# Kernel tuning notes

Hardware: AMD Instinct MI355X
Metric: run time of the kernel (lower is better)

The kernel has to match this reference:

```python
import jax, jax.numpy as jnp
import numpy as np
import math

NPAD = 100      # npadding
NLAYERS = 4     # transformer_num_layers
NHEAD = 8       # transformer_nhead


def _posenc(T, d):
    pos = jnp.arange(T, dtype=jnp.float32)[:, None]
    div = jnp.exp(jnp.arange(0, d, 2, dtype=jnp.float32) * (-(math.log(1000.0) / d)))
    pe = jnp.zeros((T, d), jnp.float32)
    pe = pe.at[:, 0::2].set(jnp.sin(pos * div))
    pe = pe.at[:, 1::2].set(jnp.cos(pos * div))
    return pe


def _ln(x, g, b):
    m = x.mean(-1, keepdims=True)
    v = ((x - m) ** 2).mean(-1, keepdims=True)
    return (x - m) / jnp.sqrt(v + 1e-5) * g + b


def conv_individual(Y, kernel, npadding):
    # Y: (B,N,Ttot); kernel: (ntau,N). Causal zero-pad then FFT conv (faithful to source).
    B, N, Ttot = Y.shape
    kernel = jnp.concatenate([jnp.zeros((1, N), kernel.dtype), kernel], axis=0)
    ntau = kernel.shape[0]
    nn = Ttot + ntau - 1
    Yf = jnp.fft.fft(Y, n=nn, axis=2)                 # (B,N,nn) complex
    Kf = jnp.fft.fft(kernel.T, n=nn, axis=-1)          # (N,nn)
    c = jnp.fft.ifft(Yf * Kf[None], axis=2).real
    c = jnp.where(jnp.abs(c) < 1e-5, 0.0, c)           # ad-hoc small-value zeroing from source
    return c[:, :, :Ttot][:, :, npadding:]             # (B,N,T)


def conv_subspace(Y, kernel, npadding):
    # Y: (B,N,Ttot); kernel: (ntau,S) -> G: (B,N,S,T)
    B, N, Ttot = Y.shape
    k = kernel[None]                                   # (1,ntau,S)
    k = jnp.concatenate([jnp.zeros((1, 1, k.shape[2]), jnp.float32), k], axis=1)
    ntau = k.shape[1]
    nn = Ttot + ntau - 1
    Yf = jnp.fft.fft(Y, n=nn, axis=2)[..., None]       # (B,N,nn,1)
    Kf = jnp.fft.fft(k, n=nn, axis=1)[None]            # (1,1,nn,S)
    G = jnp.fft.ifft(Yf * Kf, axis=2).real             # (B,N,nn,S)
    G = jnp.where(jnp.abs(G) < 1e-5, 0.0, G)
    G = G[:, :, :Ttot, :][:, :, npadding:, :]
    return jnp.swapaxes(G, -1, -2)                     # (B,N,S,T)


def _encoder(x, Wqkv, bqkv, Wo, bo, ln1_g, ln1_b, W1, b1, W2, b2, ln2_g, ln2_b):
    B, T, D = x.shape
    hd = D // NHEAD
    for l in range(NLAYERS):
        qkv = x @ Wqkv[l] + bqkv[l]                    # (B,T,3D)
        q, k, v = jnp.split(qkv, 3, axis=-1)
        q = q.reshape(B, T, NHEAD, hd)
        k = k.reshape(B, T, NHEAD, hd)
        v = v.reshape(B, T, NHEAD, hd)
        scores = jnp.einsum('bthd,bshd->bhts', q, k) / jnp.sqrt(jnp.float32(hd))
        attn = jax.nn.softmax(scores, axis=-1)
        o = jnp.einsum('bhts,bshd->bthd', attn, v).reshape(B, T, D)
        x = _ln(x + (o @ Wo[l] + bo[l]), ln1_g[l], ln1_b[l])
        ff = jax.nn.gelu(x @ W1[l] + b1[l], approximate=False) @ W2[l] + b2[l]
        x = _ln(x + ff, ln2_g[l], ln2_b[l])
    return x


def reference(Y, token_W, token_b, Wqkv, bqkv, Wo, bo, ln1_g, ln1_b, W1, b1, W2, b2,
              ln2_g, ln2_b, toL_W, toL_b, dec_W1, dec_b1, dec_W2, dec_b2,
              stimulus_basis, readout_W, coupling_W, coupling_basis, self_kernel):
    B, N, Ttot = Y.shape
    T = Ttot - NPAD
    D = token_W.shape[1]
    # token conversion over time (seq dim = time)
    x = jnp.swapaxes(Y[:, :, NPAD:], 1, 2) @ token_W + token_b   # (B,T,D)
    x = x + _posenc(T, D)[None]
    x = _encoder(x, Wqkv, bqkv, Wo, bo, ln1_g, ln1_b, W1, b1, W2, b2, ln2_g, ln2_b)
    pooled = x.mean(axis=1)                                      # (B,D)
    h = pooled @ toL_W + toL_b                                   # (B,2Z)
    Z = h.shape[1] // 2
    z = h[:, :Z]                                                 # mu (sample_latent=False)
    # stimulus decoder (2-layer MLP)
    coeffs = jax.nn.relu(z @ dec_W1 + dec_b1) @ dec_W2 + dec_b2  # (B, NF*NB)
    NB = stimulus_basis.shape[1]
    NF = coeffs.shape[1] // NB
    coeffs = coeffs.reshape(B, NF, NB)
    sti_lat = jnp.einsum('bfk,tk->bft', coeffs, stimulus_basis)  # (B,NF,T)
    sti = jnp.einsum('nf,bft->bnt', readout_W, sti_lat)          # (B,N,T)
    # coupling via FFT causal conv into subspaces
    G = conv_subspace(Y, coupling_basis, NPAD)                   # (B,N,S,T)
    cpl = jnp.einsum('ns,bnst->bnt', coupling_W, G)
    # self-history FFT causal conv
    slf = conv_individual(Y, self_kernel, NPAD)
    return sti + cpl + slf                                       # log firing rate (B,N,T)


def setup_inputs() -> dict:
    key = jax.random.key(0)
    ks = jax.random.split(key, 30)
    B, N, Ttot = 16, 256, 1100
    D, FF, Zdim = 256, 1024, 64
    NB, NF, S, NTAU = 30, 4, 4, 20   # NF = narea*stimulus_nfactor = 2*2
    T = Ttot - NPAD
    sc = 0.02
    inp = {
        'Y': jax.random.uniform(ks[0], (B, N, Ttot), jnp.float32),
        'token_W': jax.random.normal(ks[1], (N, D), jnp.float32) * sc,
        'token_b': jnp.zeros((D,), jnp.float32),
        'Wqkv': jax.random.normal(ks[2], (NLAYERS, D, 3 * D), jnp.float32) * sc,
        'bqkv': jnp.zeros((NLAYERS, 3 * D), jnp.float32),
        'Wo': jax.random.normal(ks[3], (NLAYERS, D, D), jnp.float32) * sc,
        'bo': jnp.zeros((NLAYERS, D), jnp.float32),
        'ln1_g': jnp.ones((NLAYERS, D), jnp.float32),
        'ln1_b': jnp.zeros((NLAYERS, D), jnp.float32),
        'W1': jax.random.normal(ks[4], (NLAYERS, D, FF), jnp.float32) * sc,
        'b1': jnp.zeros((NLAYERS, FF), jnp.float32),
        'W2': jax.random.normal(ks[5], (NLAYERS, FF, D), jnp.float32) * sc,
        'b2': jnp.zeros((NLAYERS, D), jnp.float32),
        'ln2_g': jnp.ones((NLAYERS, D), jnp.float32),
        'ln2_b': jnp.zeros((NLAYERS, D), jnp.float32),
        'toL_W': jax.random.normal(ks[6], (D, 2 * Zdim), jnp.float32) * sc,
        'toL_b': jnp.zeros((2 * Zdim,), jnp.float32),
        'dec_W1': jax.random.normal(ks[7], (Zdim, 2 * Zdim), jnp.float32) * sc,
        'dec_b1': jnp.zeros((2 * Zdim,), jnp.float32),
        'dec_W2': jax.random.normal(ks[8], (2 * Zdim, NB * NF), jnp.float32) * sc * 0.001,
        'dec_b2': jnp.zeros((NB * NF,), jnp.float32),
        'stimulus_basis': jax.random.normal(ks[9], (T, NB), jnp.float32),
        'readout_W': jax.random.normal(ks[10], (N, NF), jnp.float32) * sc,
        'coupling_W': jax.random.normal(ks[11], (N, S), jnp.float32) * sc,
        'coupling_basis': jax.random.normal(ks[12], (NTAU, S), jnp.float32) * 0.1,
        'self_kernel': jax.random.normal(ks[13], (NTAU, N), jnp.float32) * 0.1,
    }
    return inp
```

## Files before the change

kernel.cpp:

```cpp
#include <hip/hip_runtime.h>
#include <math.h>

#define TT_   1000
#define TTOT_ 1100
#define NPAD_ 100
#define DD_   256
#define NN_   256

#define X_OFF    0u
#define XB_OFF   4096000u
#define O_OFF    6144000u
#define R_OFF    8192000u
#define BIG_OFF  12288000u
#define WT_OFF   20480000u
#define PE_OFF   22085632u
#define PP_OFF   22341632u
#define PL_OFF   (PP_OFF + 32768u)
#define CF_OFF   (PL_OFF + 4096u)
#define CB_OFF   (CF_OFF + 1920u)
#define BQ_OFF   (CB_OFF + 5120u)
#define STL_OFF  (BQ_OFF + 3072u)

#define SC2_ 0.25503902254649546f

typedef __attribute__((ext_vector_type(8))) short s16x8;
typedef __attribute__((ext_vector_type(4))) float f32x4;
typedef __attribute__((ext_vector_type(16))) float f32x16;
typedef __attribute__((ext_vector_type(4))) unsigned u32x4;

__device__ inline short f2bf(float f) {
    unsigned u = __float_as_uint(f);
    u += 0x7fffu + ((u >> 16) & 1u);
    return (short)(u >> 16);
}
__device__ inline float exp2i(float x) {
    float r; asm("v_exp_f32 %0, %1" : "=v"(r) : "v"(x)); return r;
}

__device__ inline void gl_lds16(const short* g, short* l) {
    __builtin_amdgcn_global_load_lds(
        (const __attribute__((address_space(1))) void*)g,
        (__attribute__((address_space(3))) void*)l, 16, 0, 0);
}

__global__ __launch_bounds__(256) void wtr_k(const float* __restrict__ in,
                                             short* __restrict__ out, int K, int N,
                                             int qrows, float qs)
{
    __shared__ float t[32][33];
    const int n0 = blockIdx.x * 32, k0 = blockIdx.y * 32;
    in  += (size_t)blockIdx.z * K * N;
    out += (size_t)blockIdx.z * K * N;
    const int tx = threadIdx.x & 31, ty = threadIdx.x >> 5;
    #pragma unroll
    for (int i = 0; i < 4; ++i)
        t[ty + 8 * i][tx] = in[(size_t)(k0 + ty + 8 * i) * N + n0 + tx];
    __syncthreads();
    #pragma unroll
    for (int i = 0; i < 4; ++i) {
        const int row = n0 + ty + 8 * i;
        float f = t[tx][ty + 8 * i];
        if (row < qrows) f *= qs;
        out[(size_t)row * K + k0 + tx] = f2bf(f);
    }
}

__global__ __launch_bounds__(256) void ytr_k(const float* __restrict__ Y,
                                             short* __restrict__ out)
{
    __shared__ float t[32][33];
    const int b = blockIdx.z;
    const int t0 = blockIdx.x * 32, n0 = blockIdx.y * 32;
    const int tx = threadIdx.x & 31, ty = threadIdx.x >> 5;
    #pragma unroll
    for (int i = 0; i < 4; ++i) {
        const int tt = t0 + tx;
        t[ty + 8 * i][tx] = (tt < TT_)
            ? Y[((size_t)(b * NN_ + n0 + ty + 8 * i)) * TTOT_ + NPAD_ + tt] : 0.f;
    }
    __syncthreads();
    #pragma unroll
    for (int i = 0; i < 4; ++i) {
        const int tt = t0 + ty + 8 * i;
        if (tt < TT_)
            out[((size_t)(b * TT_ + tt)) * NN_ + n0 + tx] = f2bf(t[tx][ty + 8 * i]);
    }
}

__global__ void pe_k(float* __restrict__ PE)
{
    const int t = blockIdx.x, d = threadIdx.x;
    const float div = __expf(-(float)(d & ~1) * 0.0269834190585241f);
    const float ang = (float)t * div;
    PE[t * 256 + d] = (d & 1) ? cosf(ang) : sinf(ang);
}

__global__ void bscale_k(const float* __restrict__ in, float* __restrict__ out)
{
    const int i = blockIdx.x * 256 + threadIdx.x;
    if (i < 3072) {
        const int col = i % 768;
        out[i] = in[i] * ((col < 256) ? SC2_ : 1.f);
    }
}

template<int OUTBF, int ACT, int RES, int DUAL>
__global__ __launch_bounds__(256) void bgemm_k(const short* __restrict__ A,
                                               const short* __restrict__ Bt,
                                               const float* __restrict__ bias,
                                               const float* __restrict__ resid,
                                               void* __restrict__ Cout,
                                               short* __restrict__ Cb,
                                               int M, int N, int K, int nby)
{
    __shared__ short As[64 * 64];
    __shared__ short Bs[128 * 64];
    const int tid = threadIdx.x;

    const int nwg = gridDim.x;
    int gid = blockIdx.x;
    {
        const int q = nwg >> 3, r = nwg & 7;
        const int x = gid & 7, idx = gid >> 3;
        gid = (x < r ? x * (q + 1) : r * (q + 1) + (x - r) * q) + idx;
    }
    const int bx = gid / nby, by = gid - bx * nby;
    const int m0 = bx * 64, n0 = by * 128;

    const int wv = tid >> 6, lane = tid & 63;
    const int wr = wv >> 1, wc = wv & 1;
    const int l15 = lane & 15, lg = lane >> 4;

    f32x4 acc[2][4];
    #pragma unroll
    for (int i = 0; i < 2; ++i)
        #pragma unroll
        for (int j = 0; j < 4; ++j) acc[i][j] = (f32x4){0.f, 0.f, 0.f, 0.f};

    const int nt = K >> 6;
    for (int t = 0; t < nt; ++t) {
        __syncthreads();
        const int k0 = t << 6;
        #pragma unroll
        for (int i = 0; i < 2; ++i) {
            const int cid = i * 256 + tid;
            const int r = cid >> 3, c = cid & 7;
            gl_lds16(A + (size_t)(m0 + r) * K + k0 + ((c ^ (r & 7)) * 8), As + cid * 8);
        }
        #pragma unroll
        for (int i = 0; i < 4; ++i) {
            const int cid = i * 256 + tid;
            const int r = cid >> 3, c = cid & 7;
            gl_lds16(Bt + (size_t)(n0 + r) * K + k0 + ((c ^ (r & 7)) * 8), Bs + cid * 8);
        }
        __syncthreads();

        #pragma unroll
        for (int ks = 0; ks < 2; ++ks) {
            s16x8 af[2], bf[4];
            #pragma unroll
            for (int mi = 0; mi < 2; ++mi) {
                const int row = wr * 32 + mi * 16 + l15;
                const int ch = ks * 4 + lg;
                af[mi] = *(const s16x8*)(As + row * 64 + ((ch ^ (row & 7)) * 8));
            }
            #pragma unroll
            for (int ni = 0; ni < 4; ++ni) {
                const int col = wc * 64 + ni * 16 + l15;
                const int ch = ks * 4 + lg;
                bf[ni] = *(const s16x8*)(Bs + col * 64 + ((ch ^ (col & 7)) * 8));
            }
            #pragma unroll
            for (int mi = 0; mi < 2; ++mi)
                #pragma unroll
                for (int ni = 0; ni < 4; ++ni)
                    acc[mi][ni] = __builtin_amdgcn_mfma_f32_16x16x32_bf16(
                        af[mi], bf[ni], acc[mi][ni], 0, 0, 0);
        }
    }

    #pragma unroll
    for (int mi = 0; mi < 2; ++mi) {
        #pragma unroll
        for (int ni = 0; ni < 4; ++ni) {
            const int col = n0 + wc * 64 + ni * 16 + l15;
            const float bv = bias[col];
            #pragma unroll
            for (int r = 0; r < 4; ++r) {
                const int row = m0 + wr * 32 + mi * 16 + lg * 4 + r;
                float v = acc[mi][ni][r] + bv;
                if (RES == 1) v += resid[(size_t)row * N + col];
                if (RES == 2) v += resid[(size_t)(row % 1000) * N + col];
                if (ACT) v = 0.5f * v * (1.0f + erff(v * 0.70710678118654752f));
                if (OUTBF) ((short*)Cout)[(size_t)row * N + col] = f2bf(v);
                else       ((float*)Cout)[(size_t)row * N + col] = v;
                if (DUAL)  Cb[(size_t)row * N + col] = f2bf(v);
            }
        }
    }
}

__global__ __launch_bounds__(256) void mattn_k(const short* __restrict__ qkv,
                                               short* __restrict__ o)
{
    int wg = blockIdx.x;
    wg = (wg & 7) * 128 + (wg >> 3);
    const int qt = wg & 7, h = (wg >> 3) & 7, b = wg >> 6;

    const int tid = threadIdx.x, wv = tid >> 6, lane = tid & 63;
    const int q31 = lane & 31, hi = lane >> 5;
    __shared__ short Ks[2][64 * 40];
    __shared__ short VT[2][32 * 72];

    const int q0w = qt * 128 + wv * 32;
    int qrow = q0w + q31; if (qrow > 999) qrow = 999;
    s16x8 bq[2];
    #pragma unroll
    for (int dh = 0; dh < 2; ++dh)
        bq[dh] = *(const s16x8*)(qkv + ((size_t)(b * TT_ + qrow)) * 768 + h * 32 + dh * 16 + hi * 8);

    f32x16 oacc;
    #pragma unroll
    for (int i = 0; i < 16; ++i) oacc[i] = 0.f;
    float lrun = 0.f;

    const int sr = tid >> 2, sc = tid & 3;
    s16x8 kreg, vreg;
    auto LOADT = [&](int kt) {
        int t = kt * 64 + sr; if (t > 999) t = 999;
        const short* src = qkv + ((size_t)(b * TT_ + t)) * 768 + 256 + h * 32;
        kreg = *(const s16x8*)(src + sc * 8);
        vreg = *(const s16x8*)(src + 256 + sc * 8);
    };
    auto WRITET = [&](int buf) {
        *(s16x8*)(&Ks[buf][sr * 40 + sc * 8]) = kreg;
        #pragma unroll
        for (int j = 0; j < 8; ++j)
            VT[buf][(sc * 8 + j) * 72 + (((sr >> 3) ^ sc) * 8) + (sr & 7)] = vreg[j];
    };

    LOADT(0); WRITET(0);
    __syncthreads();
    int cur = 0;

    for (int kt = 0; kt < 16; ++kt) {
        if (kt < 15) LOADT(kt + 1);

        f32x16 st[2];
        __builtin_amdgcn_s_setprio(1);
        #pragma unroll
        for (int kb = 0; kb < 2; ++kb) {
            s16x8 kf0 = *(const s16x8*)(&Ks[cur][(kb * 32 + q31) * 40 + hi * 8]);
            s16x8 kf1 = *(const s16x8*)(&Ks[cur][(kb * 32 + q31) * 40 + 16 + hi * 8]);
            f32x16 z;
            #pragma unroll
            for (int i = 0; i < 16; ++i) z[i] = 0.f;
            z = __builtin_amdgcn_mfma_f32_32x32x16_bf16(kf0, bq[0], z, 0, 0, 0);
            z = __builtin_amdgcn_mfma_f32_32x32x16_bf16(kf1, bq[1], z, 0, 0, 0);
            st[kb] = z;
        }
        __builtin_amdgcn_s_setprio(0);

        if (kt == 15) {
            #pragma unroll
            for (int kb = 0; kb < 2; ++kb)
                #pragma unroll
                for (int r = 0; r < 16; ++r) {
                    const int kloc = kb * 32 + (r & 3) + 8 * (r >> 2) + 4 * hi;
                    if (960 + kloc >= TT_) st[kb][r] = -1e30f;
                }
        }

        float sloc = 0.f;
        #pragma unroll
        for (int kb = 0; kb < 2; ++kb)
            #pragma unroll
            for (int r = 0; r < 16; ++r) {
                const float p = exp2i(st[kb][r]);
                st[kb][r] = p; sloc += p;
            }
        sloc += __shfl_xor(sloc, 32);
        lrun += sloc;

        unsigned wk[2][4][2];
        #pragma unroll
        for (int kb = 0; kb < 2; ++kb)
            #pragma unroll
            for (int a = 0; a < 4; ++a)
                #pragma unroll
                for (int h2 = 0; h2 < 2; ++h2) {
                    unsigned rr;
                    asm("v_cvt_pk_bf16_f32 %0, %1, %2"
                        : "=v"(rr)
                        : "v"(st[kb][4 * a + 2 * h2]), "v"(st[kb][4 * a + 2 * h2 + 1]));
                    wk[kb][a][h2] = rr;
                }

        #pragma unroll
        for (int ks = 0; ks < 4; ++ks) {
            const int kb = ks >> 1, qq = ks & 1;
            unsigned W[4];
            #pragma unroll
            for (int h2 = 0; h2 < 2; ++h2) {
                const unsigned send = hi ? wk[kb][2 * qq][h2] : wk[kb][2 * qq + 1][h2];
                const unsigned recv = __shfl_xor(send, 32);
                W[h2]     = hi ? recv : wk[kb][2 * qq][h2];
                W[2 + h2] = hi ? wk[kb][2 * qq + 1][h2] : recv;
            }
            u32x4 w4 = (u32x4){W[0], W[1], W[2], W[3]};
            s16x8 pb = __builtin_bit_cast(s16x8, w4);
            s16x8 vf = *(const s16x8*)(&VT[cur][q31 * 72 + (((2 * ks + hi) ^ (q31 >> 3)) * 8)]);
            __builtin_amdgcn_s_setprio(1);
            oacc = __builtin_amdgcn_mfma_f32_32x32x16_bf16(vf, pb, oacc, 0, 0, 0);
            __builtin_amdgcn_s_setprio(0);
        }

        if (kt < 15) WRITET(cur ^ 1);
        __syncthreads();
        cur ^= 1;
    }

    const int t = q0w + q31;
    if (t < TT_) {
        const float inv = 1.f / lrun;
        short* ob = o + ((size_t)(b * TT_ + t)) * 256 + h * 32;
        #pragma unroll
        for (int a = 0; a < 4; ++a) {
            unsigned w0, w1;
            asm("v_cvt_pk_bf16_f32 %0, %1, %2"
                : "=v"(w0) : "v"(oacc[4 * a + 0] * inv), "v"(oacc[4 * a + 1] * inv));
            asm("v_cvt_pk_bf16_f32 %0, %1, %2"
                : "=v"(w1) : "v"(oacc[4 * a + 2] * inv), "v"(oacc[4 * a + 3] * inv));
            const int d0 = 8 * a + 4 * hi;
            *(unsigned*)(ob + d0) = w0;
            *(unsigned*)(ob + d0 + 2) = w1;
        }
    }
}

__global__ __launch_bounds__(256) void ln_k(const float* __restrict__ in,
                                            const float* __restrict__ g,
                                            const float* __restrict__ b,
                                            float* __restrict__ out,
                                            short* __restrict__ outb)
{
    const int row = blockIdx.x * 4 + (threadIdx.x >> 6);
    const int lane = threadIdx.x & 63;
    const size_t base = (size_t)row * 256 + lane * 4;
    float4 v = *(const float4*)(in + base);
    float s = v.x + v.y + v.z + v.w;
    #pragma unroll
    for (int msk = 1; msk < 64; msk <<= 1) s += __shfl_xor(s, msk);
    const float mean = s * (1.f / 256.f);
    float4 d; d.x = v.x - mean; d.y = v.y - mean; d.z = v.z - mean; d.w = v.w - mean;
    float q = d.x * d.x + d.y * d.y + d.z * d.z + d.w * d.w;
    #pragma unroll
    for (int msk = 1; msk < 64; msk <<= 1) q += __shfl_xor(q, msk);
    const float rs = rsqrtf(q * (1.f / 256.f) + 1e-5f);
    const float4 g4 = *(const float4*)(g + lane * 4);
    const float4 b4 = *(const float4*)(b + lane * 4);
    float4 o4;
    o4.x = d.x * rs * g4.x + b4.x;
    o4.y = d.y * rs * g4.y + b4.y;
    o4.z = d.z * rs * g4.z + b4.z;
    o4.w = d.w * rs * g4.w + b4.w;
    *(float4*)(out + base) = o4;
    short4 s4;
    s4.x = f2bf(o4.x); s4.y = f2bf(o4.y); s4.z = f2bf(o4.z); s4.w = f2bf(o4.w);
    *(short4*)(outb + base) = s4;
}

__global__ __launch_bounds__(256) void pool_part_k(const float* __restrict__ X,
                                                   float* __restrict__ partial)
{
    const int b = blockIdx.x, seg = blockIdx.y, d = threadIdx.x;
    float s = 0.f;
    const int t0 = seg * 125;
    for (int t = t0; t < t0 + 125; ++t) s += X[((size_t)b * TT_ + t) * 256 + d];
    partial[(b * 8 + seg) * 256 + d] = s;
}
__global__ __launch_bounds__(256) void pool_red_k(const float* __restrict__ partial,
                                                  float* __restrict__ pooled)
{
    const int b = blockIdx.x, d = threadIdx.x;
    float s = 0.f;
    for (int k = 0; k < 8; ++k) s += partial[(b * 8 + k) * 256 + d];
    pooled[b * 256 + d] = s * (1.f / (float)TT_);
}

__global__ __launch_bounds__(128) void head_k(const float* __restrict__ pooled,
                                              const float* __restrict__ toLW,
                                              const float* __restrict__ toLb,
                                              const float* __restrict__ dW1,
                                              const float* __restrict__ db1,
                                              const float* __restrict__ dW2,
                                              const float* __restrict__ db2,
                                              float* __restrict__ coeffs)
{
    const int b = blockIdx.x, j = threadIdx.x;
    __shared__ float hs[64];
    __shared__ float hid[128];
    float a = toLb[j];
    for (int d = 0; d < 256; ++d) a += pooled[b * 256 + d] * toLW[d * 128 + j];
    if (j < 64) hs[j] = a;
    __syncthreads();
    float a2 = db1[j];
    for (int z = 0; z < 64; ++z) a2 += hs[z] * dW1[z * 128 + j];
    hid[j] = fmaxf(a2, 0.f);
    __syncthreads();
    if (j < 120) {
        float a3 = db2[j];
        for (int k = 0; k < 128; ++k) a3 += hid[k] * dW2[k * 120 + j];
        coeffs[b * 120 + j] = a3;
    }
}

__global__ void comb_k(const float* __restrict__ selfK,
                       const float* __restrict__ cplW,
                       const float* __restrict__ cplB,
                       float* __restrict__ comb)
{
    const int n = threadIdx.x;
    for (int ti = 0; ti < 20; ++ti) {
        float s = selfK[ti * 256 + n];
        #pragma unroll
        for (int si = 0; si < 4; ++si) s += cplW[n * 4 + si] * cplB[ti * 4 + si];
        comb[n * 20 + ti] = s;
    }
}

__global__ __launch_bounds__(256) void stilat_k(const float* __restrict__ SB,
                                                const float* __restrict__ coeffs,
                                                float* __restrict__ STL)
{
    const int bf = blockIdx.x;
    __shared__ float c[30];
    if (threadIdx.x < 30) c[threadIdx.x] = coeffs[(bf >> 2) * 120 + (bf & 3) * 30 + threadIdx.x];
    __syncthreads();
    for (int t = threadIdx.x; t < TT_; t += 256) {
        float acc = 0.f;
        const float* sp = SB + (size_t)t * 30;
        #pragma unroll
        for (int k = 0; k < 30; ++k) acc += c[k] * sp[k];
        STL[bf * TT_ + t] = acc;
    }
}

__global__ __launch_bounds__(256) void final_k(const float* __restrict__ Y,
                                               const float* __restrict__ STL,
                                               const float* __restrict__ roW,
                                               const float* __restrict__ comb,
                                               float* __restrict__ out)
{
    const int bx = blockIdx.x;
    const int ts = bx & 3, nc = (bx >> 2) & 31, b = bx >> 7;
    const int n0 = nc * 8, t0 = ts * 250;
    const int tid = threadIdx.x;
    __shared__ float rw[8][4], ck[8][20], yl[8][272];

    if (tid < 32) rw[tid >> 2][tid & 3] = roW[(n0 + (tid >> 2)) * 4 + (tid & 3)];
    if (tid >= 64 && tid < 224) {
        const int j = tid - 64;
        ck[j / 20][j % 20] = comb[(n0 + j / 20) * 20 + (j % 20)];
    }
    for (int j = tid; j < 2160; j += 256) {
        const int n = j / 270, jj = j - n * 270;
        yl[n][jj] = Y[((size_t)(b * 256 + n0 + n)) * TTOT_ + t0 + 80 + jj];
    }
    __syncthreads();

    if (tid < 250) {
        const int t = t0 + tid;
        float s4[4];
        #pragma unroll
        for (int f = 0; f < 4; ++f) s4[f] = STL[((size_t)b * 4 + f) * TT_ + t];
        #pragma unroll
        for (int n = 0; n < 8; ++n) {
            float acc = rw[n][0] * s4[0] + rw[n][1] * s4[1]
                      + rw[n][2] * s4[2] + rw[n][3] * s4[3];
            #pragma unroll
            for (int tau = 1; tau <= 20; ++tau)
                acc += ck[n][tau - 1] * yl[n][tid + 20 - tau];
            out[((size_t)(b * 256 + n0 + n)) * TT_ + t] = acc;
        }
    }
}

extern "C" void kernel_launch(void* const* d_in, const int* in_sizes, int n_in,
                              void* d_out, int out_size, void* d_ws, size_t ws_size,
                              hipStream_t stream)
{
    const float* Y      = (const float*)d_in[0];
    const float* tokW   = (const float*)d_in[1];
    const float* tokb   = (const float*)d_in[2];
    const float* Wqkv   = (const float*)d_in[3];
    const float* bqkv   = (const float*)d_in[4];
    const float* Wo     = (const float*)d_in[5];
    const float* bo     = (const float*)d_in[6];
    const float* ln1g   = (const float*)d_in[7];
    const float* ln1b   = (const float*)d_in[8];
    const float* W1     = (const float*)d_in[9];
    const float* b1     = (const float*)d_in[10];
    const float* W2     = (const float*)d_in[11];
    const float* b2     = (const float*)d_in[12];
    const float* ln2g   = (const float*)d_in[13];
    const float* ln2b   = (const float*)d_in[14];
    const float* toLW   = (const float*)d_in[15];
    const float* toLb   = (const float*)d_in[16];
    const float* dW1    = (const float*)d_in[17];
    const float* db1    = (const float*)d_in[18];
    const float* dW2    = (const float*)d_in[19];
    const float* db2    = (const float*)d_in[20];
    const float* SB     = (const float*)d_in[21];
    const float* roW    = (const float*)d_in[22];
    const float* cplW   = (const float*)d_in[23];
    const float* cplB   = (const float*)d_in[24];
    const float* selfK  = (const float*)d_in[25];

    float* ws  = (float*)d_ws;
    float* X   = ws + X_OFF;
    short* Xb  = (short*)(ws + XB_OFF);
    short* O   = (short*)(ws + O_OFF);
    float* R   = ws + R_OFF;
    short* BIG = (short*)(ws + BIG_OFF);
    short* WT  = (short*)(ws + WT_OFF);
    float* PE  = ws + PE_OFF;
    float* PP  = ws + PP_OFF;
    float* PL  = ws + PL_OFF;
    float* CF  = ws + CF_OFF;
    float* CB  = ws + CB_OFF;
    float* BQ  = ws + BQ_OFF;
    float* STL = ws + STL_OFF;

    short* WTqkv = WT;
    short* WTo   = WT + 786432;
    short* WTw1  = WT + 1048576;
    short* WTw2  = WT + 2097152;
    short* WTtok = WT + 3145728;
    short* Ybt   = BIG;

    wtr_k<<<dim3(24, 8, 4), 256, 0, stream>>>(Wqkv, WTqkv, 256, 768, 256, SC2_);
    wtr_k<<<dim3(8, 8, 4),  256, 0, stream>>>(Wo,   WTo,   256, 256, 0, 1.f);
    wtr_k<<<dim3(32, 8, 4), 256, 0, stream>>>(W1,   WTw1,  256, 1024, 0, 1.f);
    wtr_k<<<dim3(8, 32, 4), 256, 0, stream>>>(W2,   WTw2,  1024, 256, 0, 1.f);
    wtr_k<<<dim3(8, 8, 1),  256, 0, stream>>>(tokW, WTtok, 256, 256, 0, 1.f);
    bscale_k<<<12, 256, 0, stream>>>(bqkv, BQ);
    pe_k<<<1000, 256, 0, stream>>>(PE);
    ytr_k<<<dim3(32, 8, 16), 256, 0, stream>>>(Y, Ybt);

    bgemm_k<0, 0, 2, 1><<<500, 256, 0, stream>>>(
        Ybt, WTtok, tokb, PE, X, Xb, 16000, 256, 256, 2);

    for (int l = 0; l < 4; ++l) {
        bgemm_k<1, 0, 0, 0><<<1500, 256, 0, stream>>>(
            Xb, WTqkv + (size_t)l * 196608, BQ + l * 768, nullptr, BIG, nullptr,
            16000, 768, 256, 6);
        mattn_k<<<1024, 256, 0, stream>>>(BIG, O);
        bgemm_k<0, 0, 1, 0><<<500, 256, 0, stream>>>(
            O, WTo + (size_t)l * 65536, bo + l * 256, X, R, nullptr,
            16000, 256, 256, 2);
        ln_k<<<4000, 256, 0, stream>>>(R, ln1g + l * 256, ln1b + l * 256, X, Xb);
        bgemm_k<1, 1, 0, 0><<<2000, 256, 0, stream>>>(
            Xb, WTw1 + (size_t)l * 262144, b1 + l * 1024, nullptr, BIG, nullptr,
            16000, 1024, 256, 8);
        bgemm_k<0, 0, 1, 0><<<500, 256, 0, stream>>>(
            BIG, WTw2 + (size_t)l * 262144, b2 + l * 256, X, R, nullptr,
            16000, 256, 1024, 2);
        ln_k<<<4000, 256, 0, stream>>>(R, ln2g + l * 256, ln2b + l * 256, X, Xb);
    }

    pool_part_k<<<dim3(16, 8), 256, 0, stream>>>(X, PP);
    pool_red_k<<<16, 256, 0, stream>>>(PP, PL);
    head_k<<<16, 128, 0, stream>>>(PL, toLW, toLb, dW1, db1, dW2, db2, CF);
    comb_k<<<1, 256, 0, stream>>>(selfK, cplW, cplB, CB);
    stilat_k<<<64, 256, 0, stream>>>(SB, CF, STL);
    final_k<<<2048, 256, 0, stream>>>(Y, STL, roW, CB, (float*)d_out);
}
```

Before: 554.3 us.

## Add 128x128 GEMM tile for QKV/FFN1 and move softmax row sums to MFMA

Adds a bgemm128_k kernel with 128x128 output tiles, XOR-swizzled LDS staging and 16x16x32 bf16 MFMA. It replaces the smaller-tile GEMM for the QKV and FFN1 projections, aiming for more operand reuse per LDS load and fewer workgroups. In attention, the softmax denominator is now computed by an extra MFMA against a ones vector instead of scalar adds plus a shuffle. V is loaded as pairs of rows and written to the transposed LDS tile with packed 32-bit stores instead of single 16-bit scalar stores. The trade-offs are higher register pressure from the 4x4 accumulators and extra MFMA work in the attention loop.

```diff
diff --git a/kernel.cpp b/kernel.cpp
--- a/kernel.cpp
+++ b/kernel.cpp
@@ -200,6 +200,91 @@
     }
 }
 
+template<int ACT>
+__global__ __launch_bounds__(256) void bgemm128_k(const short* __restrict__ A,
+                                                  const short* __restrict__ Bt,
+                                                  const float* __restrict__ bias,
+                                                  short* __restrict__ Cout,
+                                                  int M, int N, int K, int nby)
+{
+    __shared__ short As[128 * 64];
+    __shared__ short Bs[128 * 64];
+    const int tid = threadIdx.x;
+
+    const int nwg = gridDim.x;
+    int gid = blockIdx.x;
+    {
+        const int q = nwg >> 3, r = nwg & 7;
+        const int x = gid & 7, idx = gid >> 3;
+        gid = (x < r ? x * (q + 1) : r * (q + 1) + (x - r) * q) + idx;
+    }
+    const int bx = gid / nby, by = gid - bx * nby;
+    const int m0 = bx * 128, n0 = by * 128;
+
+    const int wv = tid >> 6, lane = tid & 63;
+    const int wr = wv >> 1, wc = wv & 1;
+    const int l15 = lane & 15, lg = lane >> 4;
+
+    f32x4 acc[4][4];
+    #pragma unroll
+    for (int i = 0; i < 4; ++i)
+        #pragma unroll
+        for (int j = 0; j < 4; ++j) acc[i][j] = (f32x4){0.f, 0.f, 0.f, 0.f};
+
+    const int nt = K >> 6;
+    for (int t = 0; t < nt; ++t) {
+        __syncthreads();
+        const int k0 = t << 6;
+        #pragma unroll
+        for (int i = 0; i < 4; ++i) {
+            const int cid = i * 256 + tid;
+            const int r = cid >> 3, c = cid & 7;
+            gl_lds16(A + (size_t)(m0 + r) * K + k0 + ((c ^ (r & 7)) * 8), As + cid * 8);
+            gl_lds16(Bt + (size_t)(n0 + r) * K + k0 + ((c ^ (r & 7)) * 8), Bs + cid * 8);
+        }
+        __syncthreads();
+
+        #pragma unroll
+        for (int ks = 0; ks < 2; ++ks) {
+            s16x8 af[4], bf[4];
+            #pragma unroll
+            for (int mi = 0; mi < 4; ++mi) {
+                const int row = wr * 64 + mi * 16 + l15;
+                const int ch = ks * 4 + lg;
+                af[mi] = *(const s16x8*)(As + row * 64 + ((ch ^ (row & 7)) * 8));
+            }
+            #pragma unroll
+            for (int ni = 0; ni < 4; ++ni) {
+                const int col = wc * 64 + ni * 16 + l15;
+                const int ch = ks * 4 + lg;
+                bf[ni] = *(const s16x8*)(Bs + col * 64 + ((ch ^ (col & 7)) * 8));
+            }
+            #pragma unroll
+            for (int mi = 0; mi < 4; ++mi)
+                #pragma unroll
+                for (int ni = 0; ni < 4; ++ni)
+                    acc[mi][ni] = __builtin_amdgcn_mfma_f32_16x16x32_bf16(
+                        af[mi], bf[ni], acc[mi][ni], 0, 0, 0);
+        }
+    }
+
+    #pragma unroll
+    for (int mi = 0; mi < 4; ++mi) {
+        #pragma unroll
+        for (int ni = 0; ni < 4; ++ni) {
+            const int col = n0 + wc * 64 + ni * 16 + l15;
+            const float bv = bias[col];
+            #pragma unroll
+            for (int r = 0; r < 4; ++r) {
+                const int row = m0 + wr * 64 + mi * 16 + lg * 4 + r;
+                float v = acc[mi][ni][r] + bv;
+                if (ACT) v = 0.5f * v * (1.0f + erff(v * 0.70710678118654752f));
+                Cout[(size_t)row * N + col] = f2bf(v);
+            }
+        }
+    }
+}
+
 __global__ __launch_bounds__(256) void mattn_k(const short* __restrict__ qkv,
                                                short* __restrict__ o)
 {
@@ -219,24 +304,38 @@
     for (int dh = 0; dh < 2; ++dh)
         bq[dh] = *(const s16x8*)(qkv + ((size_t)(b * TT_ + qrow)) * 768 + h * 32 + dh * 16 + hi * 8);
 
-    f32x16 oacc;
-    #pragma unroll
-    for (int i = 0; i < 16; ++i) oacc[i] = 0.f;
-    float lrun = 0.f;
+    s16x8 ones;
+    #pragma unroll
+    for (int i = 0; i < 8; ++i) ones[i] = (short)0x3F80;
+
+    f32x16 oacc, lacc;
+    #pragma unroll
+    for (int i = 0; i < 16; ++i) { oacc[i] = 0.f; lacc[i] = 0.f; }
 
     const int sr = tid >> 2, sc = tid & 3;
-    s16x8 kreg, vreg;
+    const int kp = tid >> 3, dq = (tid & 7) * 4;
+    s16x8 kreg;
+    short4 va, vb;
     auto LOADT = [&](int kt) {
         int t = kt * 64 + sr; if (t > 999) t = 999;
-        const short* src = qkv + ((size_t)(b * TT_ + t)) * 768 + 256 + h * 32;
-        kreg = *(const s16x8*)(src + sc * 8);
-        vreg = *(const s16x8*)(src + 256 + sc * 8);
+        kreg = *(const s16x8*)(qkv + ((size_t)(b * TT_ + t)) * 768 + 256 + h * 32 + sc * 8);
+        int t0 = kt * 64 + 2 * kp, t1 = t0 + 1;
+        if (t0 > 999) t0 = 999;
+        if (t1 > 999) t1 = 999;
+        va = *(const short4*)(qkv + ((size_t)(b * TT_ + t0)) * 768 + 512 + h * 32 + dq);
+        vb = *(const short4*)(qkv + ((size_t)(b * TT_ + t1)) * 768 + 512 + h * 32 + dq);
     };
     auto WRITET = [&](int buf) {
         *(s16x8*)(&Ks[buf][sr * 40 + sc * 8]) = kreg;
-        #pragma unroll
-        for (int j = 0; j < 8; ++j)
-            VT[buf][(sc * 8 + j) * 72 + (((sr >> 3) ^ sc) * 8) + (sr & 7)] = vreg[j];
+        const int c = kp >> 2;
+        const int ko = (2 * kp) & 7;
+        #pragma unroll
+        for (int j = 0; j < 4; ++j) {
+            const int d = dq + j;
+            const unsigned pk = ((unsigned)(unsigned short)((&va.x)[j]))
+                              | (((unsigned)(unsigned short)((&vb.x)[j])) << 16);
+            *(unsigned*)(&VT[buf][d * 72 + ((c ^ (d >> 3)) * 8) + ko]) = pk;
+        }
     };
 
     LOADT(0); WRITET(0);
@@ -271,16 +370,10 @@
                 }
         }
 
-        float sloc = 0.f;
         #pragma unroll
         for (int kb = 0; kb < 2; ++kb)
             #pragma unroll
-            for (int r = 0; r < 16; ++r) {
-                const float p = exp2i(st[kb][r]);
-                st[kb][r] = p; sloc += p;
-            }
-        sloc += __shfl_xor(sloc, 32);
-        lrun += sloc;
+            for (int r = 0; r < 16; ++r) st[kb][r] = exp2i(st[kb][r]);
 
         unsigned wk[2][4][2];
         #pragma unroll
@@ -312,6 +405,7 @@
             s16x8 vf = *(const s16x8*)(&VT[cur][q31 * 72 + (((2 * ks + hi) ^ (q31 >> 3)) * 8)]);
             __builtin_amdgcn_s_setprio(1);
             oacc = __builtin_amdgcn_mfma_f32_32x32x16_bf16(vf, pb, oacc, 0, 0, 0);
+            lacc = __builtin_amdgcn_mfma_f32_32x32x16_bf16(ones, pb, lacc, 0, 0, 0);
             __builtin_amdgcn_s_setprio(0);
         }
 
@@ -322,7 +416,7 @@
 
     const int t = q0w + q31;
     if (t < TT_) {
-        const float inv = 1.f / lrun;
+        const float inv = 1.f / lacc[0];
         short* ob = o + ((size_t)(b * TT_ + t)) * 256 + h * 32;
         #pragma unroll
         for (int a = 0; a < 4; ++a) {
@@ -552,16 +646,16 @@
         Ybt, WTtok, tokb, PE, X, Xb, 16000, 256, 256, 2);
 
     for (int l = 0; l < 4; ++l) {
-        bgemm_k<1, 0, 0, 0><<<1500, 256, 0, stream>>>(
-            Xb, WTqkv + (size_t)l * 196608, BQ + l * 768, nullptr, BIG, nullptr,
+        bgemm128_k<0><<<750, 256, 0, stream>>>(
+            Xb, WTqkv + (size_t)l * 196608, BQ + l * 768, BIG,
             16000, 768, 256, 6);
         mattn_k<<<1024, 256, 0, stream>>>(BIG, O);
         bgemm_k<0, 0, 1, 0><<<500, 256, 0, stream>>>(
             O, WTo + (size_t)l * 65536, bo + l * 256, X, R, nullptr,
             16000, 256, 256, 2);
         ln_k<<<4000, 256, 0, stream>>>(R, ln1g + l * 256, ln1b + l * 256, X, Xb);
-        bgemm_k<1, 1, 0, 0><<<2000, 256, 0, stream>>>(
-            Xb, WTw1 + (size_t)l * 262144, b1 + l * 1024, nullptr, BIG, nullptr,
+        bgemm128_k<1><<<1000, 256, 0, stream>>>(
+            Xb, WTw1 + (size_t)l * 262144, b1 + l * 1024, BIG,
             16000, 1024, 256, 8);
         bgemm_k<0, 0, 1, 0><<<500, 256, 0, stream>>>(
             BIG, WTw2 + (size_t)l * 262144, b2 + l * 256, X, R, nullptr,
```

Result: slower. 622.3 us (+12.3%).
